# Optimization experiments

Hardware: AMD Instinct MI355X
Metric: run time of the kernel (lower is better)

## Reference

```python
import jax, jax.numpy as jnp
import numpy as np

NUM_NODES = 21

def _adjacency():
    edges = [(0, r) for r in [1, 5, 9, 13, 17]]
    for fs in [1, 5, 9, 13, 17]:
        edges += [(fs, fs + 1), (fs + 1, fs + 2), (fs + 2, fs + 3)]
    A = np.zeros((NUM_NODES, NUM_NODES), dtype=np.float32)
    for i, j in edges:
        A[i, j] = 1.0
        A[j, i] = 1.0
    A = A + np.eye(NUM_NODES, dtype=np.float32)
    d_inv_sqrt = np.power(A.sum(axis=1), -0.5)
    return jnp.asarray(d_inv_sqrt[:, None] * A * d_inv_sqrt[None, :])

A_HAT = _adjacency()  # [21, 21]


def _causal_conv_relu(x, w, b, dilation):
    # x: [B, T, Cin], w: [K, Cin, Cout] ('WIO'), causal left pad (K-1)*d
    k = w.shape[0]
    y = jax.lax.conv_general_dilated(
        x, w, window_strides=(1,), padding=[((k - 1) * dilation, 0)],
        rhs_dilation=(dilation,), dimension_numbers=('NWC', 'WIO', 'NWC'))
    return jax.nn.relu(y + b)


def _mstcn(x, ws, bs, wm, bm, wl, bl, wo, bo):
    x1 = _causal_conv_relu(x, ws, bs, 1)   # k=3
    x2 = _causal_conv_relu(x, wm, bm, 2)   # k=5, d=2
    x3 = _causal_conv_relu(x, wl, bl, 4)   # k=9, d=4
    h = jnp.concatenate([x1, x2, x3], axis=-1)  # [B, T, filters]
    return jnp.einsum('btc,cd->btd', h, wo[0]) + bo  # 1x1 conv_out


def _adapter(x):
    # x: [B, T, 218] -> [B, T, 21, 18]
    B, T = x.shape[0], x.shape[1]
    palm = x[..., 0:18][:, :, None, :]                     # [B, T, 1, 18]
    bones = x[..., 18:].reshape(B, T, 20, 10)              # [B, T, 20, 10]
    bones = jnp.concatenate(
        [bones, jnp.zeros((B, T, 20, 8), dtype=x.dtype)], axis=-1)
    return jnp.concatenate([palm, bones], axis=-2)


def setup_inputs() -> dict:
    key = jax.random.key(0)
    ks = jax.random.split(key, 12)
    s = 0.05
    B, T = 16, 4096
    inp = {
        'x': jax.random.normal(ks[0], (B, T, 218), jnp.float32),
        'gcn_w': jax.random.normal(ks[1], (18, 64), jnp.float32) * s,
        'wd': jax.random.normal(ks[2], (64, 32), jnp.float32) * s,
        'bd': jnp.zeros((32,), jnp.float32),
    }
    for i, p in enumerate(['t1', 't2']):
        kk = jax.random.split(ks[3 + i], 4)
        inp[p + '_ws'] = jax.random.normal(kk[0], (3, 64, 16), jnp.float32) * s
        inp[p + '_bs'] = jnp.zeros((16,), jnp.float32)
        inp[p + '_wm'] = jax.random.normal(kk[1], (5, 64, 16), jnp.float32) * s
        inp[p + '_bm'] = jnp.zeros((16,), jnp.float32)
        inp[p + '_wl'] = jax.random.normal(kk[2], (9, 64, 32), jnp.float32) * s
        inp[p + '_bl'] = jnp.zeros((32,), jnp.float32)
        inp[p + '_wo'] = jax.random.normal(kk[3], (1, 64, 64), jnp.float32) * s
        inp[p + '_bo'] = jnp.zeros((64,), jnp.float32)
    return inp


def reference(x, gcn_w, t1_ws, t1_bs, t1_wm, t1_bm, t1_wl, t1_bl, t1_wo, t1_bo,
              t2_ws, t2_bs, t2_wm, t2_bm, t2_wl, t2_bl, t2_wo, t2_bo, wd, bd):
    g = _adapter(x)                                   # [B, T, 21, 18]
    h = jnp.einsum('btvc,cd->btvd', g, gcn_w)         # node-wise projection
    h = jnp.einsum('vw,btwd->btvd', A_HAT, h)         # graph propagation
    h = jax.nn.relu(h)
    h_pool = jnp.mean(h, axis=2)                      # [B, T, 64]
    t1 = _mstcn(h_pool, t1_ws, t1_bs, t1_wm, t1_bm, t1_wl, t1_bl, t1_wo, t1_bo)
    t2 = _mstcn(t1, t2_ws, t2_bs, t2_wm, t2_bm, t2_wl, t2_bl, t2_wo, t2_bo)
    out = jnp.tanh(jnp.einsum('btc,cd->btd', t2, wd) + bd)  # [B, T, 32]
    return jnp.mean(out, axis=1)                      # [B, 32]
```

## Files before the change

### kernel.cpp

```cpp
#include <hip/hip_runtime.h>
#include <hip/hip_bf16.h>
#include <math.h>

#define T_LEN 4096
#define BATCH 16

typedef _Float16 f16;
typedef _Float16 f16x2 __attribute__((ext_vector_type(2)));
typedef _Float16 f16x8 __attribute__((ext_vector_type(8)));
typedef float f32x4 __attribute__((ext_vector_type(4)));

__device__ __align__(16) f16 g_pk[132 * 1024];

__global__ void k_pack(
    const float* __restrict__ ws1, const float* __restrict__ wm1,
    const float* __restrict__ wl1, const float* __restrict__ wo1,
    const float* __restrict__ ws2, const float* __restrict__ wm2,
    const float* __restrict__ wl2, const float* __restrict__ wo2,
    const float* __restrict__ wd,  const float* __restrict__ gcn_w)
{
    const int g = blockIdx.x;
    const int tid = threadIdx.x;
    #pragma unroll
    for (int u = 0; u < 2; ++u) {
        const int e = tid * 2 + u;
        const int lane = e >> 3, j = e & 7;
        const int m = lane & 15, k = (lane >> 4) * 8 + j;
        float w;
        if (g < 120) {
            const int layer = g / 60, r0 = g % 60;
            const float* pws = layer ? ws2 : ws1;
            const float* pwm = layer ? wm2 : wm1;
            const float* pwl = layer ? wl2 : wl1;
            const float* pwo = layer ? wo2 : wo1;
            if (r0 < 6) {
                const int kp = r0 >> 1, q = r0 & 1;
                w = pws[(kp * 64 + q * 32 + k) * 16 + m];
            } else if (r0 < 16) {
                const int r = r0 - 6, kp = r >> 1, q = r & 1;
                w = pwm[(kp * 64 + q * 32 + k) * 16 + m];
            } else if (r0 < 52) {
                const int r = r0 - 16, kp = r >> 2, q = (r >> 1) & 1, ms = r & 1;
                w = pwl[(kp * 64 + q * 32 + k) * 32 + ms * 16 + m];
            } else {
                const int r = r0 - 52, ms = r >> 1, kh = r & 1;
                w = pwo[(kh * 32 + k) * 64 + ms * 16 + m];
            }
        } else if (g < 124) {
            const int r = g - 120, ms = r >> 1, kh = r & 1;
            w = wd[(kh * 32 + k) * 32 + ms * 16 + m];
        } else {
            const int r = g - 124, df = r & 3;
            const int lim = (r >> 2) ? 18 : 10;
            w = (k < lim) ? gcn_w[k * 64 + df * 16 + m] : 0.f;
        }
        const f16 hi = (f16)w;
        const f16 lo = (f16)(w - (float)hi);
        g_pk[g * 1024 + e] = hi;
        g_pk[g * 1024 + 512 + e] = lo;
    }
}

__device__ inline f32x4 mfma3z(f16x8 ah, f16x8 al, f16x8 bh, f16x8 bl) {
    f32x4 a = {0.f, 0.f, 0.f, 0.f};
    a = __builtin_amdgcn_mfma_f32_16x16x32_f16(ah, bh, a, 0, 0, 0);
    a = __builtin_amdgcn_mfma_f32_16x16x32_f16(ah, bl, a, 0, 0, 0);
    a = __builtin_amdgcn_mfma_f32_16x16x32_f16(al, bh, a, 0, 0, 0);
    return a;
}

__global__ __launch_bounds__(256) void k_gcn(
    const float* __restrict__ x,
    float* __restrict__ hp)
{
    __shared__ __align__(16) float xt[64 * 220];

    const int b   = blockIdx.y;
    const int t0  = blockIdx.x * 64;
    const int tid = threadIdx.x;

    {
        const float* xb = x + ((long)b * T_LEN + t0) * 218;
        #pragma unroll 1
        for (int i = tid; i < 64 * 109; i += 256) {
            const int row = i / 109;
            const int c = (i - row * 109) * 2;
            *(float2*)(&xt[row * 220 + c]) = *(const float2*)(xb + row * 218 + c);
        }
    }
    __syncthreads();

    const int lane = tid & 63, wid = tid >> 6;
    const int l15 = lane & 15, lg = lane >> 4;
    const int t = t0 + wid * 16 + l15;
    const float* xrow = xt + (wid * 16 + l15) * 220;
    const int la8 = lane * 8;

    const float cP = 1.0f / 6.0f;
    const float cS = 0.23570226039551584f;
    const float c3 = 1.0f / 3.0f;
    const float cT = 0.4082482904638631f;
    const float cH = 0.5f;

    f32x4 h0[4];
    {
        float vv[8];
        const int po = (lg < 2) ? lg * 8 : 16;
        *(float4*)(vv + 0) = *(const float4*)(xrow + po);
        *(float4*)(vv + 4) = *(const float4*)(xrow + po + 4);
        f16x8 bh, bl;
        #pragma unroll
        for (int j = 0; j < 8; ++j) {
            const f16 h = (f16)vv[j];
            bh[j] = h; bl[j] = (f16)(vv[j] - (float)h);
        }
        #pragma unroll
        for (int df = 0; df < 4; ++df) {
            const f16x8 ah = *(const f16x8*)(g_pk + (128 + df) * 1024 + la8);
            const f16x8 al = *(const f16x8*)(g_pk + (128 + df) * 1024 + 512 + la8);
            h0[df] = mfma3z(ah, al, bh, bl);
        }
    }

    f16x8 Abh[4], Abl[4];
    #pragma unroll
    for (int df = 0; df < 4; ++df) {
        Abh[df] = *(const f16x8*)(g_pk + (124 + df) * 1024 + la8);
        Abl[df] = *(const f16x8*)(g_pk + (124 + df) * 1024 + 512 + la8);
    }

    f32x4 pool[4], star[4], s12[4], hprev[4];
    #pragma unroll
    for (int df = 0; df < 4; ++df) {
        pool[df] = (f32x4){0.f, 0.f, 0.f, 0.f};
        star[df] = (f32x4){0.f, 0.f, 0.f, 0.f};
    }

    #pragma unroll 1
    for (int f = 0; f < 5; ++f) {
        #pragma unroll
        for (int n = 0; n < 4; ++n) {
            const int w = 4 * f + n;
            const float* bp = xrow + 18 + 10 * w;
            float vv[8];
            const bool g0 = (lg == 0);
            *(float2*)(vv + 0) = *(const float2*)(bp + ((lg == 1) ? 8 : 0));
            *(float2*)(vv + 2) = *(const float2*)(bp + (g0 ? 2 : 0));
            *(float2*)(vv + 4) = *(const float2*)(bp + (g0 ? 4 : 0));
            *(float2*)(vv + 6) = *(const float2*)(bp + (g0 ? 6 : 0));
            f16x8 bh, bl;
            #pragma unroll
            for (int j = 0; j < 8; ++j) {
                const f16 h = (f16)vv[j];
                bh[j] = h; bl[j] = (f16)(vv[j] - (float)h);
            }
            f32x4 hn[4];
            #pragma unroll
            for (int df = 0; df < 4; ++df)
                hn[df] = mfma3z(Abh[df], Abl[df], bh, bl);

            #pragma unroll
            for (int df = 0; df < 4; ++df)
                #pragma unroll
                for (int i = 0; i < 4; ++i) {
                    const float h = hn[df][i];
                    if (n == 0) {
                        star[df][i] += h;
                        s12[df][i] = h;
                        hprev[df][i] = h;
                    } else if (n == 1) {
                        const float pa = fmaf(cS, h0[df][i], c3 * (s12[df][i] + h));
                        pool[df][i] += fmaxf(pa, 0.f);
                        s12[df][i] += h;
                        hprev[df][i] = h;
                    } else if (n == 2) {
                        const float pb = c3 * (s12[df][i] + h);
                        pool[df][i] += fmaxf(pb, 0.f);
                        s12[df][i] = hprev[df][i] + h;
                        hprev[df][i] = h;
                    } else {
                        const float pc = fmaf(cT, h, c3 * s12[df][i]);
                        const float pe = fmaf(cT, hprev[df][i], cH * h);
                        pool[df][i] += fmaxf(pc, 0.f) + fmaxf(pe, 0.f);
                    }
                }
        }
    }

    float* hpb = hp + (long)b * 64 * T_LEN + t;
    #pragma unroll
    for (int df = 0; df < 4; ++df)
        #pragma unroll
        for (int i = 0; i < 4; ++i) {
            const float p0 = fmaf(cP, h0[df][i], cS * star[df][i]);
            hpb[(long)(df * 16 + lg * 4 + i) * T_LEN] =
                (pool[df][i] + fmaxf(p0, 0.f)) * (1.0f / 21.0f);
        }
}

template <bool FINAL>
__global__ __launch_bounds__(512, 4) void k_mstcn(
    const float* __restrict__ in,
    const float* __restrict__ bs, const float* __restrict__ bm,
    const float* __restrict__ bl, const float* __restrict__ bo,
    int pkoff,
    float* __restrict__ out,
    const float* __restrict__ bd,
    float* __restrict__ outp)
{
    __shared__ __align__(16) f16 lds[34816];

    const int b   = blockIdx.y;
    const int t0  = blockIdx.x * 128;
    const int tid = threadIdx.x;
    const float* inb = in + (long)b * 64 * T_LEN;

    {
        const int c0 = (tid >> 4) * 2;
        const int tq = (tid & 15) * 10;
        float v0[10], v1[10];
        if (t0 != 0 || tq >= 40) {
            const float* r0 = inb + (long)c0 * T_LEN + (t0 - 32 + tq);
            const float* r1 = r0 + T_LEN;
            #pragma unroll
            for (int m = 0; m < 5; ++m) {
                *(float2*)(v0 + 2 * m) = *(const float2*)(r0 + 2 * m);
                *(float2*)(v1 + 2 * m) = *(const float2*)(r1 + 2 * m);
            }
        } else {
            #pragma unroll
            for (int i = 0; i < 10; ++i) {
                const int tg_ = tq + i - 32;
                v0[i] = (tg_ >= 0) ? inb[(long)c0 * T_LEN + tg_] : 0.f;
                v1[i] = (tg_ >= 0) ? inb[(long)(c0 + 1) * T_LEN + tg_] : 0.f;
            }
        }
        #pragma unroll
        for (int i = 0; i < 10; ++i) {
            const int row = tq + i;
            const f16 h0 = (f16)v0[i], h1 = (f16)v1[i];
            *(f16x2*)(&lds[row * 72 + c0]) = (f16x2){h0, h1};
            *(f16x2*)(&lds[11520 + row * 72 + c0]) =
                (f16x2){(f16)(v0[i] - (float)h0), (f16)(v1[i] - (float)h1)};
        }
    }
    __syncthreads();

    const int lane = tid & 63, wid = tid >> 6;
    const int qh  = wid >> 2;
    const int tg  = wid & 3;
    const int l15 = lane & 15, lg = lane >> 4;
    const int tws0 = tg * 32, tws1 = tg * 32 + 16;
    const f16* pk = g_pk + pkoff;
    const int la8 = lane * 8;

#define MFMA3(ACC, AH, AL, BH, BL) do {                                    \
        ACC = __builtin_amdgcn_mfma_f32_16x16x32_f16(AH, BH, ACC, 0,0,0);  \
        ACC = __builtin_amdgcn_mfma_f32_16x16x32_f16(AH, BL, ACC, 0,0,0);  \
        ACC = __builtin_amdgcn_mfma_f32_16x16x32_f16(AL, BH, ACC, 0,0,0);  \
    } while (0)

#define LOADA(AH, AL, FR) do {                                             \
        AH = *(const f16x8*)(pk + (FR) * 1024 + la8);                      \
        AL = *(const f16x8*)(pk + (FR) * 1024 + 512 + la8);                \
    } while (0)

#define BRD(BH, BL, ROW) do {                                              \
        const int r_ = (ROW);                                              \
        BH = *(const f16x8*)(&lds[r_ * 72 + qh * 32 + lg * 8]);            \
        BL = *(const f16x8*)(&lds[11520 + r_ * 72 + qh * 32 + lg * 8]);    \
    } while (0)

    f32x4 aS0 = {0.f,0.f,0.f,0.f}, aS1 = {0.f,0.f,0.f,0.f};
    f32x4 aM0 = {0.f,0.f,0.f,0.f}, aM1 = {0.f,0.f,0.f,0.f};
    f32x4 aL00 = {0.f,0.f,0.f,0.f}, aL01 = {0.f,0.f,0.f,0.f};
    f32x4 aL10 = {0.f,0.f,0.f,0.f}, aL11 = {0.f,0.f,0.f,0.f};

    #pragma unroll
    for (int kp = 0; kp < 3; ++kp) {
        f16x8 ah, al, bh, bv;
        LOADA(ah, al, 2 * kp + qh);
        BRD(bh, bv, 30 + tws0 + l15 + kp); MFMA3(aS0, ah, al, bh, bv);
        BRD(bh, bv, 30 + tws1 + l15 + kp); MFMA3(aS1, ah, al, bh, bv);
    }
    #pragma unroll
    for (int kp = 0; kp < 5; ++kp) {
        f16x8 ah, al, bh, bv;
        LOADA(ah, al, 6 + 2 * kp + qh);
        BRD(bh, bv, 24 + tws0 + l15 + 2 * kp); MFMA3(aM0, ah, al, bh, bv);
        BRD(bh, bv, 24 + tws1 + l15 + 2 * kp); MFMA3(aM1, ah, al, bh, bv);
    }
    #pragma unroll
    for (int kp = 0; kp < 9; ++kp) {
        f16x8 a0h, a0l, a1h, a1l, bh, bv;
        LOADA(a0h, a0l, 16 + 4 * kp + 2 * qh);
        LOADA(a1h, a1l, 16 + 4 * kp + 2 * qh + 1);
        BRD(bh, bv, tws0 + l15 + 4 * kp);
        MFMA3(aL00, a0h, a0l, bh, bv); MFMA3(aL10, a1h, a1l, bh, bv);
        BRD(bh, bv, tws1 + l15 + 4 * kp);
        MFMA3(aL01, a0h, a0l, bh, bv); MFMA3(aL11, a1h, a1l, bh, bv);
    }

    __syncthreads();
    {
        float* red = (float*)lds;
        const int ro = (tg * 64 + lane) * 4;
        if (qh == 0) {
            *(f32x4*)(red + 0 * 1024 + ro) = aS0;
            *(f32x4*)(red + 1 * 1024 + ro) = aM0;
            *(f32x4*)(red + 2 * 1024 + ro) = aL00;
            *(f32x4*)(red + 3 * 1024 + ro) = aL10;
            *(f32x4*)(red + 4 * 1024 + ro) = aS1;
            *(f32x4*)(red + 5 * 1024 + ro) = aM1;
            *(f32x4*)(red + 6 * 1024 + ro) = aL01;
            *(f32x4*)(red + 7 * 1024 + ro) = aL11;
        }
        __syncthreads();
        if (qh == 0) return;
        aS0  += *(const f32x4*)(red + 0 * 1024 + ro);
        aM0  += *(const f32x4*)(red + 1 * 1024 + ro);
        aL00 += *(const f32x4*)(red + 2 * 1024 + ro);
        aL10 += *(const f32x4*)(red + 3 * 1024 + ro);
        aS1  += *(const f32x4*)(red + 4 * 1024 + ro);
        aM1  += *(const f32x4*)(red + 5 * 1024 + ro);
        aL01 += *(const f32x4*)(red + 6 * 1024 + ro);
        aL11 += *(const f32x4*)(red + 7 * 1024 + ro);
    }

#define STAGEH(ACC, BPTR, JB, RELU, RB) do {                               \
        const float4 bv_ = *(const float4*)(BPTR);                         \
        float x0_ = ACC[0] + bv_.x, x1_ = ACC[1] + bv_.y,                  \
              x2_ = ACC[2] + bv_.z, x3_ = ACC[3] + bv_.w;                  \
        if (RELU) { x0_ = fmaxf(x0_, 0.f); x1_ = fmaxf(x1_, 0.f);          \
                    x2_ = fmaxf(x2_, 0.f); x3_ = fmaxf(x3_, 0.f); }        \
        const f16 h0_ = (f16)x0_, h1_ = (f16)x1_;                          \
        const f16 h2_ = (f16)x2_, h3_ = (f16)x3_;                          \
        const int ro_ = ((RB) + l15) * 72 + (JB) + lg * 4;                 \
        *(f16x2*)(&lds[16384 + ro_])     = (f16x2){h0_, h1_};              \
        *(f16x2*)(&lds[16384 + ro_ + 2]) = (f16x2){h2_, h3_};              \
        *(f16x2*)(&lds[25600 + ro_])     =                                 \
            (f16x2){(f16)(x0_ - (float)h0_), (f16)(x1_ - (float)h1_)};     \
        *(f16x2*)(&lds[25600 + ro_ + 2]) =                                 \
            (f16x2){(f16)(x2_ - (float)h2_), (f16)(x3_ - (float)h3_)};     \
    } while (0)

    STAGEH(aS0,  bs + lg * 4,       0,  true, tws0);
    STAGEH(aM0,  bm + lg * 4,       16, true, tws0);
    STAGEH(aL00, bl + lg * 4,       32, true, tws0);
    STAGEH(aL10, bl + 16 + lg * 4,  48, true, tws0);
    STAGEH(aS1,  bs + lg * 4,       0,  true, tws1);
    STAGEH(aM1,  bm + lg * 4,       16, true, tws1);
    STAGEH(aL01, bl + lg * 4,       32, true, tws1);
    STAGEH(aL11, bl + 16 + lg * 4,  48, true, tws1);

#define HRD(BH, BL, RB, KH) do {                                           \
        const int ro_ = ((RB) + l15) * 72 + (KH) * 32 + lg * 8;            \
        BH = *(const f16x8*)(&lds[16384 + ro_]);                           \
        BL = *(const f16x8*)(&lds[25600 + ro_]);                           \
    } while (0)

    f32x4 oA0 = {0.f,0.f,0.f,0.f}, oA1 = {0.f,0.f,0.f,0.f};
    f32x4 oA2 = {0.f,0.f,0.f,0.f}, oA3 = {0.f,0.f,0.f,0.f};
    f32x4 oB0 = {0.f,0.f,0.f,0.f}, oB1 = {0.f,0.f,0.f,0.f};
    f32x4 oB2 = {0.f,0.f,0.f,0.f}, oB3 = {0.f,0.f,0.f,0.f};
    #pragma unroll
    for (int kh = 0; kh < 2; ++kh) {
        f16x8 b0h, b0l, b1h, b1l, ah, al;
        HRD(b0h, b0l, tws0, kh);
        HRD(b1h, b1l, tws1, kh);
        LOADA(ah, al, 52 + 0 + kh);
        MFMA3(oA0, ah, al, b0h, b0l); MFMA3(oB0, ah, al, b1h, b1l);
        LOADA(ah, al, 52 + 2 + kh);
        MFMA3(oA1, ah, al, b0h, b0l); MFMA3(oB1, ah, al, b1h, b1l);
        LOADA(ah, al, 52 + 4 + kh);
        MFMA3(oA2, ah, al, b0h, b0l); MFMA3(oB2, ah, al, b1h, b1l);
        LOADA(ah, al, 52 + 6 + kh);
        MFMA3(oA3, ah, al, b0h, b0l); MFMA3(oB3, ah, al, b1h, b1l);
    }

    if (!FINAL) {
        const float4 b0v = *(const float4*)(bo + lg * 4);
        const float4 b1v = *(const float4*)(bo + 16 + lg * 4);
        const float4 b2v = *(const float4*)(bo + 32 + lg * 4);
        const float4 b3v = *(const float4*)(bo + 48 + lg * 4);
#define STO4(ACC, BV, MS, OB) do {                                         \
        (OB)[((MS) * 16 + lg * 4 + 0) * (long)T_LEN] = ACC[0] + BV.x;      \
        (OB)[((MS) * 16 + lg * 4 + 1) * (long)T_LEN] = ACC[1] + BV.y;      \
        (OB)[((MS) * 16 + lg * 4 + 2) * (long)T_LEN] = ACC[2] + BV.z;      \
        (OB)[((MS) * 16 + lg * 4 + 3) * (long)T_LEN] = ACC[3] + BV.w;      \
    } while (0)
        float* obA = out + (long)b * 64 * T_LEN + t0 + tws0 + l15;
        float* obB = out + (long)b * 64 * T_LEN + t0 + tws1 + l15;
        STO4(oA0, b0v, 0, obA); STO4(oB0, b0v, 0, obB);
        STO4(oA1, b1v, 1, obA); STO4(oB1, b1v, 1, obB);
        STO4(oA2, b2v, 2, obA); STO4(oB2, b2v, 2, obB);
        STO4(oA3, b3v, 3, obA); STO4(oB3, b3v, 3, obB);
#undef STO4
    } else {
        STAGEH(oA0, bo + lg * 4,       0,  false, tws0);
        STAGEH(oA1, bo + 16 + lg * 4,  16, false, tws0);
        STAGEH(oA2, bo + 32 + lg * 4,  32, false, tws0);
        STAGEH(oA3, bo + 48 + lg * 4,  48, false, tws0);
        STAGEH(oB0, bo + lg * 4,       0,  false, tws1);
        STAGEH(oB1, bo + 16 + lg * 4,  16, false, tws1);
        STAGEH(oB2, bo + 32 + lg * 4,  32, false, tws1);
        STAGEH(oB3, bo + 48 + lg * 4,  48, false, tws1);

        f32x4 eA0 = {0.f,0.f,0.f,0.f}, eA1 = {0.f,0.f,0.f,0.f};
        f32x4 eB0 = {0.f,0.f,0.f,0.f}, eB1 = {0.f,0.f,0.f,0.f};
        #pragma unroll
        for (int kh = 0; kh < 2; ++kh) {
            f16x8 b0h, b0l, b1h, b1l, ah, al;
            HRD(b0h, b0l, tws0, kh);
            HRD(b1h, b1l, tws1, kh);
            ah = *(const f16x8*)(g_pk + (120 + 0 + kh) * 1024 + la8);
            al = *(const f16x8*)(g_pk + (120 + 0 + kh) * 1024 + 512 + la8);
            MFMA3(eA0, ah, al, b0h, b0l); MFMA3(eB0, ah, al, b1h, b1l);
            ah = *(const f16x8*)(g_pk + (120 + 2 + kh) * 1024 + la8);
            al = *(const f16x8*)(g_pk + (120 + 2 + kh) * 1024 + 512 + la8);
            MFMA3(eA1, ah, al, b0h, b0l); MFMA3(eB1, ah, al, b1h, b1l);
        }
        const float4 bd0 = *(const float4*)(bd + lg * 4);
        const float4 bd1 = *(const float4*)(bd + 16 + lg * 4);
        const float cI = 1.0f / (float)T_LEN;
        float u0 = (tanhf(eA0[0] + bd0.x) + tanhf(eB0[0] + bd0.x)) * cI;
        float u1 = (tanhf(eA0[1] + bd0.y) + tanhf(eB0[1] + bd0.y)) * cI;
        float u2 = (tanhf(eA0[2] + bd0.z) + tanhf(eB0[2] + bd0.z)) * cI;
        float u3 = (tanhf(eA0[3] + bd0.w) + tanhf(eB0[3] + bd0.w)) * cI;
        float u4 = (tanhf(eA1[0] + bd1.x) + tanhf(eB1[0] + bd1.x)) * cI;
        float u5 = (tanhf(eA1[1] + bd1.y) + tanhf(eB1[1] + bd1.y)) * cI;
        float u6 = (tanhf(eA1[2] + bd1.z) + tanhf(eB1[2] + bd1.z)) * cI;
        float u7 = (tanhf(eA1[3] + bd1.w) + tanhf(eB1[3] + bd1.w)) * cI;
#define RED(U) do { U += __shfl_xor(U, 1); U += __shfl_xor(U, 2);          \
                    U += __shfl_xor(U, 4); U += __shfl_xor(U, 8); } while (0)
        RED(u0); RED(u1); RED(u2); RED(u3);
        RED(u4); RED(u5); RED(u6); RED(u7);
#undef RED
        if (l15 == 0) {
            float* op = outp + b * 32;
            atomicAdd(op + lg * 4 + 0, u0);
            atomicAdd(op + lg * 4 + 1, u1);
            atomicAdd(op + lg * 4 + 2, u2);
            atomicAdd(op + lg * 4 + 3, u3);
            atomicAdd(op + 16 + lg * 4 + 0, u4);
            atomicAdd(op + 16 + lg * 4 + 1, u5);
            atomicAdd(op + 16 + lg * 4 + 2, u6);
            atomicAdd(op + 16 + lg * 4 + 3, u7);
        }
    }
#undef HRD
#undef STAGEH
#undef BRD
#undef LOADA
#undef MFMA3
}

extern "C" void kernel_launch(void* const* d_in, const int* in_sizes, int n_in,
                              void* d_out, int out_size, void* d_ws, size_t ws_size,
                              hipStream_t stream) {
    const float* x     = (const float*)d_in[0];
    const float* gcn_w = (const float*)d_in[1];
    const float* wd    = (const float*)d_in[2];
    const float* bd    = (const float*)d_in[3];
    const float* t1_ws = (const float*)d_in[4];
    const float* t1_bs = (const float*)d_in[5];
    const float* t1_wm = (const float*)d_in[6];
    const float* t1_bm = (const float*)d_in[7];
    const float* t1_wl = (const float*)d_in[8];
    const float* t1_bl = (const float*)d_in[9];
    const float* t1_wo = (const float*)d_in[10];
    const float* t1_bo = (const float*)d_in[11];
    const float* t2_ws = (const float*)d_in[12];
    const float* t2_bs = (const float*)d_in[13];
    const float* t2_wm = (const float*)d_in[14];
    const float* t2_bm = (const float*)d_in[15];
    const float* t2_wl = (const float*)d_in[16];
    const float* t2_bl = (const float*)d_in[17];
    const float* t2_wo = (const float*)d_in[18];
    const float* t2_bo = (const float*)d_in[19];

    float* b0 = (float*)d_ws;
    float* b1 = b0 + (size_t)BATCH * 64 * T_LEN;

    hipMemsetAsync(d_out, 0, (size_t)out_size * sizeof(float), stream);

    k_pack<<<dim3(132), 256, 0, stream>>>(
        t1_ws, t1_wm, t1_wl, t1_wo, t2_ws, t2_wm, t2_wl, t2_wo, wd, gcn_w);

    k_gcn<<<dim3(T_LEN / 64, BATCH), 256, 0, stream>>>(x, b0);

    k_mstcn<false><<<dim3(T_LEN / 128, BATCH), 512, 0, stream>>>(
        b0, t1_bs, t1_bm, t1_bl, t1_bo, 0,
        b1, nullptr, nullptr);

    k_mstcn<true><<<dim3(T_LEN / 128, BATCH), 512, 0, stream>>>(
        b1, t2_bs, t2_bm, t2_bl, t2_bo, 61440,
        nullptr, bd, (float*)d_out);
}
```

Measured before the change: 232.2 us.

## Transpose GCN input tile in LDS to channel-major and halve block size

```diff
diff --git a/kernel.cpp b/kernel.cpp
--- a/kernel.cpp
+++ b/kernel.cpp
@@ -69,31 +69,33 @@
     return a;
 }
 
-__global__ __launch_bounds__(256) void k_gcn(
+__global__ __launch_bounds__(128) void k_gcn(
     const float* __restrict__ x,
     float* __restrict__ hp)
 {
-    __shared__ __align__(16) float xt[64 * 220];
+    __shared__ __align__(16) float xt[218 * 36];
 
     const int b   = blockIdx.y;
-    const int t0  = blockIdx.x * 64;
+    const int t0  = blockIdx.x * 32;
     const int tid = threadIdx.x;
 
     {
         const float* xb = x + ((long)b * T_LEN + t0) * 218;
         #pragma unroll 1
-        for (int i = tid; i < 64 * 109; i += 256) {
-            const int row = i / 109;
-            const int c = (i - row * 109) * 2;
-            *(float2*)(&xt[row * 220 + c]) = *(const float2*)(xb + row * 218 + c);
+        for (int i = tid; i < 32 * 109; i += 128) {
+            const int t = i / 109;
+            const int c = (i - t * 109) * 2;
+            const float2 v = *(const float2*)(xb + t * 218 + c);
+            xt[c * 36 + t]       = v.x;
+            xt[(c + 1) * 36 + t] = v.y;
         }
     }
     __syncthreads();
 
     const int lane = tid & 63, wid = tid >> 6;
     const int l15 = lane & 15, lg = lane >> 4;
-    const int t = t0 + wid * 16 + l15;
-    const float* xrow = xt + (wid * 16 + l15) * 220;
+    const int tloc = wid * 16 + l15;
+    const int t = t0 + tloc;
     const int la8 = lane * 8;
 
     const float cP = 1.0f / 6.0f;
@@ -102,12 +104,19 @@
     const float cT = 0.4082482904638631f;
     const float cH = 0.5f;
 
+    int choff[8];
+    #pragma unroll
+    for (int j = 0; j < 8; ++j) {
+        const int sel = (lg == 0) ? j : ((lg == 1 && j < 2) ? 8 + j : 0);
+        choff[j] = sel * 36 + tloc;
+    }
+
     f32x4 h0[4];
     {
+        const int po = (lg < 2) ? lg * 8 : 16;
         float vv[8];
-        const int po = (lg < 2) ? lg * 8 : 16;
-        *(float4*)(vv + 0) = *(const float4*)(xrow + po);
-        *(float4*)(vv + 4) = *(const float4*)(xrow + po + 4);
+        #pragma unroll
+        for (int j = 0; j < 8; ++j) vv[j] = xt[(po + j) * 36 + tloc];
         f16x8 bh, bl;
         #pragma unroll
         for (int j = 0; j < 8; ++j) {
@@ -141,13 +150,10 @@
         #pragma unroll
         for (int n = 0; n < 4; ++n) {
             const int w = 4 * f + n;
-            const float* bp = xrow + 18 + 10 * w;
+            const int cb36 = (18 + 10 * w) * 36;
             float vv[8];
-            const bool g0 = (lg == 0);
-            *(float2*)(vv + 0) = *(const float2*)(bp + ((lg == 1) ? 8 : 0));
-            *(float2*)(vv + 2) = *(const float2*)(bp + (g0 ? 2 : 0));
-            *(float2*)(vv + 4) = *(const float2*)(bp + (g0 ? 4 : 0));
-            *(float2*)(vv + 6) = *(const float2*)(bp + (g0 ? 6 : 0));
+            #pragma unroll
+            for (int j = 0; j < 8; ++j) vv[j] = xt[cb36 + choff[j]];
             f16x8 bh, bl;
             #pragma unroll
             for (int j = 0; j < 8; ++j) {
@@ -487,7 +493,7 @@
     k_pack<<<dim3(132), 256, 0, stream>>>(
         t1_ws, t1_wm, t1_wl, t1_wo, t2_ws, t2_wm, t2_wl, t2_wo, wd, gcn_w);
 
-    k_gcn<<<dim3(T_LEN / 64, BATCH), 256, 0, stream>>>(x, b0);
+    k_gcn<<<dim3(T_LEN / 32, BATCH), 128, 0, stream>>>(x, b0);
 
     k_mstcn<false><<<dim3(T_LEN / 128, BATCH), 512, 0, stream>>>(
         b0, t1_bs, t1_bm, t1_bl, t1_bo, 0,
```

Result: no change. 235.7 us (+1.5%).
